# Kernel tuning notes

Measured on AMD Instinct MI355X. Metric: run time of the kernel, lower is better.

## Reference

```python
import jax, jax.numpy as jnp
import numpy as np

B, N, E = 2, 16000, 160000
NDIMS, NMEAS, NMODES = 2, 1, 128
IN_DIM, OUT_DIM, FC_DIM = 3, 1, 128
LAYERS = [64, 64, 64, 64]
INV_MIN, INV_MAX = 0.5, 2.0


def setup_inputs() -> dict:
    key = jax.random.key(0)
    ks = jax.random.split(key, 16)
    L = len(LAYERS) - 1
    C = LAYERS[0]
    scale = 1.0 / (C * C)
    u = lambda k, sh, s: jax.random.uniform(k, sh, jnp.float32, -s, s)
    inp = {}
    inp["x"] = jax.random.normal(ks[0], (B, N, IN_DIM), jnp.float32)
    inp["node_mask"] = jnp.ones((B, N, 1), jnp.int32)
    inp["nodes"] = jax.random.uniform(ks[1], (B, N, NDIMS), jnp.float32)
    inp["node_weights"] = jax.random.uniform(ks[2], (B, N, NMEAS), jnp.float32) / N
    inp["directed_edges"] = jax.random.randint(ks[3], (B, E, 2), 0, N, jnp.int32)
    inp["edge_gradient_weights"] = jax.random.normal(ks[4], (B, E, NDIMS), jnp.float32)
    inp["modes"] = jax.random.normal(ks[5], (NMODES, NDIMS, NMEAS), jnp.float32)
    # scaled_logit(1.0, 0.5, 2.0) = log(0.5/1.0)
    inp["inv_L_scale_latent"] = jnp.full((NDIMS, NMEAS), np.log((1.0 - INV_MIN) / (INV_MAX - 1.0)), jnp.float32)
    inp["fc0_W"] = u(ks[6], (C, IN_DIM), 1.0 / np.sqrt(IN_DIM))
    inp["fc0_b"] = jnp.zeros((C,), jnp.float32)
    inp["weights_c"] = u(ks[7], (L, C, C, NMODES, NMEAS), scale)
    inp["weights_s"] = u(ks[8], (L, C, C, NMODES, NMEAS), scale)
    inp["weights_0"] = u(ks[9], (L, C, C, 1, NMEAS), scale)
    inp["ws_W"] = u(ks[10], (L, C, C), 1.0 / np.sqrt(C))
    inp["ws_b"] = jnp.zeros((L, C), jnp.float32)
    inp["gws_W"] = u(ks[11], (L, C, C * NDIMS), 1.0 / np.sqrt(C * NDIMS))
    inp["gws_b"] = jnp.zeros((L, C), jnp.float32)
    inp["fc1_W"] = u(ks[12], (FC_DIM, C), 1.0 / np.sqrt(C))
    inp["fc1_b"] = jnp.zeros((FC_DIM,), jnp.float32)
    inp["fc2_W"] = u(ks[13], (OUT_DIM, FC_DIM), 1.0 / np.sqrt(FC_DIM))
    inp["fc2_b"] = jnp.zeros((OUT_DIM,), jnp.float32)
    return inp


def _forward(x, nodes, node_weights, edge_gradient_weights, modes, inv_L_scale_latent,
             fc0_W, fc0_b, weights_c, weights_s, weights_0, ws_W, ws_b, gws_W, gws_b,
             fc1_W, fc1_b, fc2_W, fc2_b, directed_edges):
    L = weights_c.shape[0]
    n = x.shape[1]
    # scaled sigmoid of latent inverse length scale
    inv_L = INV_MIN + (INV_MAX - INV_MIN) * jax.nn.sigmoid(inv_L_scale_latent)
    smodes = modes * inv_L  # [K, D, W]
    # Fourier bases over all nodes
    temp = jnp.einsum('bxd,kdw->bxkw', nodes, smodes)  # [B, N, K, W]
    bases_c, bases_s = jnp.cos(temp), jnp.sin(temp)
    bases_0 = jnp.ones(temp.shape[:2] + (1, temp.shape[-1]), temp.dtype)
    wnw = node_weights[:, :, None, :]  # [B, N, 1, W]
    wbases_c, wbases_s, wbases_0 = bases_c * wnw, bases_s * wnw, bases_0 * wnw

    tgt = directed_edges[..., 0]  # [B, E]
    src = directed_edges[..., 1]

    def grad_field(f):  # f: [B, C, N] -> [B, C*D, N]
        ft = jnp.transpose(f, (0, 2, 1))  # [B, N, C]
        f_src = jnp.take_along_axis(ft, src[..., None], axis=1)  # [B, E, C]
        f_tgt = jnp.take_along_axis(ft, tgt[..., None], axis=1)
        diff = f_src - f_tgt
        msg = jnp.einsum('bed,bec->becd', edge_gradient_weights, diff)  # [B, E, C, D]
        msg = msg.reshape(msg.shape[0], msg.shape[1], -1)  # [B, E, C*D]
        seg = jax.vmap(lambda m, t: jax.ops.segment_sum(m, t, num_segments=n))(msg, tgt)
        return jnp.transpose(seg, (0, 2, 1))  # [B, C*D, N]

    # lift: fc0 acts on channel dim
    h = jnp.einsum('oi,bni->bon', fc0_W, x) + fc0_b[None, :, None]  # [B, C, N]

    for i in range(L):
        # spectral conv with explicit bases
        x_c = jnp.einsum('bix,bxkw->bikw', h, wbases_c)
        x_s = -jnp.einsum('bix,bxkw->bikw', h, wbases_s)
        x_0 = jnp.einsum('bix,bxkw->bikw', h, wbases_0)
        f_c = jnp.einsum('bikw,iokw->bokw', x_c, weights_c[i]) - jnp.einsum('bikw,iokw->bokw', x_s, weights_s[i])
        f_s = jnp.einsum('bikw,iokw->bokw', x_s, weights_c[i]) + jnp.einsum('bikw,iokw->bokw', x_c, weights_s[i])
        f_0 = jnp.einsum('bikw,iokw->bokw', x_0, weights_0[i])
        x1 = (jnp.einsum('bokw,bxkw->box', f_0, bases_0)
              + 2 * jnp.einsum('bokw,bxkw->box', f_c, bases_c)
              - 2 * jnp.einsum('bokw,bxkw->box', f_s, bases_s))
        # pointwise linear W
        x2 = jnp.einsum('oi,bin->bon', ws_W[i], h) + ws_b[i][None, :, None]
        # differential operator D: gradient then linear
        x3 = jnp.einsum('oi,bin->bon', gws_W[i], grad_field(h)) + gws_b[i][None, :, None]
        h = x1 + x2 + x3
        if i < L - 1:
            h = jax.nn.gelu(h)

    out = jnp.transpose(h, (0, 2, 1))  # [B, N, C]
    out = jax.nn.gelu(jnp.einsum('oc,bnc->bno', fc1_W, out) + fc1_b)
    out = jnp.einsum('oc,bnc->bno', fc2_W, out) + fc2_b
    return out  # [B, N, out_dim]


def reference(x, node_mask, nodes, node_weights, directed_edges, edge_gradient_weights,
              modes, inv_L_scale_latent, fc0_W, fc0_b, weights_c, weights_s, weights_0,
              ws_W, ws_b, gws_W, gws_b, fc1_W, fc1_b, fc2_W, fc2_b):
    del node_mask  # padding mask; all-ones here, not used in the core math
    return _forward(x, nodes, node_weights, edge_gradient_weights, modes, inv_L_scale_latent,
                    fc0_W, fc0_b, weights_c, weights_s, weights_0, ws_W, ws_b, gws_W, gws_b,
                    fc1_W, fc1_b, fc2_W, fc2_b, directed_edges)
```

## Files before the change

### kernel.cpp

```cpp
#include <hip/hip_runtime.h>
#include <math.h>

#define BB 2
#define NN 16000
#define EE 160000
#define KK 128
#define CC 64
#define LL 3

typedef __attribute__((ext_vector_type(8))) short bf16x8;
typedef __attribute__((ext_vector_type(4))) float f32x4;

__device__ __forceinline__ float gelu_f(float x){
    float x3 = x * x * x;
    return 0.5f * x * (1.f + tanhf(0.7978845608028654f * (x + 0.044715f * x3)));
}
__device__ __forceinline__ ushort f2bf(float f){
    uint u = __float_as_uint(f);
    u += 0x7fff + ((u >> 16) & 1);
    return (ushort)(u >> 16);
}
__device__ __forceinline__ float bf2f(ushort h){ return __uint_as_float(((uint)h) << 16); }
__device__ __forceinline__ void fsplit(float v, ushort &hi, ushort &lo){
    hi = f2bf(v);
    lo = f2bf(v - bf2f(hi));
}
__device__ __forceinline__ uint pk2(ushort a, ushort b){ return (uint)a | ((uint)b << 16); }

__global__ __launch_bounds__(256) void k_bases(
    const float* __restrict__ nodes, const float* __restrict__ modes,
    const float* __restrict__ latent, const float* __restrict__ nw,
    ushort* __restrict__ cbh, ushort* __restrict__ cbl,
    ushort* __restrict__ sbh, ushort* __restrict__ sbl,
    ushort* __restrict__ wTh, ushort* __restrict__ wTl){
    int bid = blockIdx.x;
    int b = bid / 250, x0 = (bid % 250) * 64;
    int t = threadIdx.x;
    __shared__ float sm0[128], sm1[128], nwv[64];
    __shared__ uint tc[64][65], ts[64][65];
    if (t < 128){
        float i0 = 0.5f + 1.5f / (1.f + expf(-latent[0]));
        float i1 = 0.5f + 1.5f / (1.f + expf(-latent[1]));
        sm0[t] = modes[t*2+0] * i0;
        sm1[t] = modes[t*2+1] * i1;
    }
    if (t < 64) nwv[t] = nw[b*NN + x0 + t];
    __syncthreads();
    int xloc = t & 63;
    float n0 = nodes[((size_t)b*NN + x0 + xloc)*2 + 0];
    float n1 = nodes[((size_t)b*NN + x0 + xloc)*2 + 1];
    for (int kh = 0; kh < 2; kh++){
        int kq = t >> 6;
        #pragma unroll
        for (int j = 0; j < 16; j++){
            int kl = kq*16 + j;
            int k = kh*64 + kl;
            float tmp = n0*sm0[k] + n1*sm1[k];
            float sv, cv; sincosf(tmp, &sv, &cv);
            ushort h_, l_;
            fsplit(cv, h_, l_); tc[xloc][kl] = pk2(h_, l_);
            fsplit(sv, h_, l_); ts[xloc][kl] = pk2(h_, l_);
        }
        __syncthreads();
        {
            int q = t >> 6;
            size_t base = ((size_t)b*NN + x0 + xloc)*128 + kh*64 + q*16;
            #pragma unroll
            for (int g2 = 0; g2 < 2; g2++){
                uint u0 = tc[xloc][q*16 + g2*8 + 0], u1 = tc[xloc][q*16 + g2*8 + 1];
                uint u2 = tc[xloc][q*16 + g2*8 + 2], u3 = tc[xloc][q*16 + g2*8 + 3];
                uint u4 = tc[xloc][q*16 + g2*8 + 4], u5 = tc[xloc][q*16 + g2*8 + 5];
                uint u6 = tc[xloc][q*16 + g2*8 + 6], u7 = tc[xloc][q*16 + g2*8 + 7];
                uint4 vh, vl;
                vh.x = pk2((ushort)u0,(ushort)u1); vh.y = pk2((ushort)u2,(ushort)u3);
                vh.z = pk2((ushort)u4,(ushort)u5); vh.w = pk2((ushort)u6,(ushort)u7);
                vl.x = pk2((ushort)(u0>>16),(ushort)(u1>>16)); vl.y = pk2((ushort)(u2>>16),(ushort)(u3>>16));
                vl.z = pk2((ushort)(u4>>16),(ushort)(u5>>16)); vl.w = pk2((ushort)(u6>>16),(ushort)(u7>>16));
                *(uint4*)&cbh[base + g2*8] = vh;
                *(uint4*)&cbl[base + g2*8] = vl;
                u0 = ts[xloc][q*16 + g2*8 + 0]; u1 = ts[xloc][q*16 + g2*8 + 1];
                u2 = ts[xloc][q*16 + g2*8 + 2]; u3 = ts[xloc][q*16 + g2*8 + 3];
                u4 = ts[xloc][q*16 + g2*8 + 4]; u5 = ts[xloc][q*16 + g2*8 + 5];
                u6 = ts[xloc][q*16 + g2*8 + 6]; u7 = ts[xloc][q*16 + g2*8 + 7];
                vh.x = pk2((ushort)u0,(ushort)u1); vh.y = pk2((ushort)u2,(ushort)u3);
                vh.z = pk2((ushort)u4,(ushort)u5); vh.w = pk2((ushort)u6,(ushort)u7);
                vl.x = pk2((ushort)(u0>>16),(ushort)(u1>>16)); vl.y = pk2((ushort)(u2>>16),(ushort)(u3>>16));
                vl.z = pk2((ushort)(u4>>16),(ushort)(u5>>16)); vl.w = pk2((ushort)(u6>>16),(ushort)(u7>>16));
                *(uint4*)&sbh[base + g2*8] = vh;
                *(uint4*)&sbl[base + g2*8] = vl;
            }
        }
        {
            int k = t & 63, g = t >> 6;
            int kgc = kh*64 + k;
            int kgs = 128 + kh*64 + k;
            ushort hc[16], lc[16], hs[16], ls[16];
            #pragma unroll
            for (int j = 0; j < 16; j++){
                int xx = g*16 + j;
                float wgt = nwv[xx];
                uint uc = tc[xx][k], us = ts[xx][k];
                float vc = (bf2f((ushort)uc) + bf2f((ushort)(uc>>16))) * wgt;
                float vs = (bf2f((ushort)us) + bf2f((ushort)(us>>16))) * wgt;
                fsplit(vc, hc[j], lc[j]);
                fsplit(vs, hs[j], ls[j]);
            }
            size_t wbc = ((size_t)b*256 + kgc)*16000 + x0 + g*16;
            size_t wbs = ((size_t)b*256 + kgs)*16000 + x0 + g*16;
            uint4 v;
            v.x = pk2(hc[0],hc[1]); v.y = pk2(hc[2],hc[3]); v.z = pk2(hc[4],hc[5]); v.w = pk2(hc[6],hc[7]);
            *(uint4*)&wTh[wbc] = v;
            v.x = pk2(hc[8],hc[9]); v.y = pk2(hc[10],hc[11]); v.z = pk2(hc[12],hc[13]); v.w = pk2(hc[14],hc[15]);
            *(uint4*)&wTh[wbc + 8] = v;
            v.x = pk2(lc[0],lc[1]); v.y = pk2(lc[2],lc[3]); v.z = pk2(lc[4],lc[5]); v.w = pk2(lc[6],lc[7]);
            *(uint4*)&wTl[wbc] = v;
            v.x = pk2(lc[8],lc[9]); v.y = pk2(lc[10],lc[11]); v.z = pk2(lc[12],lc[13]); v.w = pk2(lc[14],lc[15]);
            *(uint4*)&wTl[wbc + 8] = v;
            v.x = pk2(hs[0],hs[1]); v.y = pk2(hs[2],hs[3]); v.z = pk2(hs[4],hs[5]); v.w = pk2(hs[6],hs[7]);
            *(uint4*)&wTh[wbs] = v;
            v.x = pk2(hs[8],hs[9]); v.y = pk2(hs[10],hs[11]); v.z = pk2(hs[12],hs[13]); v.w = pk2(hs[14],hs[15]);
            *(uint4*)&wTh[wbs + 8] = v;
            v.x = pk2(ls[0],ls[1]); v.y = pk2(ls[2],ls[3]); v.z = pk2(ls[4],ls[5]); v.w = pk2(ls[6],ls[7]);
            *(uint4*)&wTl[wbs] = v;
            v.x = pk2(ls[8],ls[9]); v.y = pk2(ls[10],ls[11]); v.z = pk2(ls[12],ls[13]); v.w = pk2(ls[14],ls[15]);
            *(uint4*)&wTl[wbs + 8] = v;
        }
        __syncthreads();
    }
}

__device__ __forceinline__ void write_h_outputs(
    const float* ot, const float* nws, int b, int s, int x0, int t, int doAux,
    float* __restrict__ hx, ushort* __restrict__ hxh, ushort* __restrict__ hxl,
    ushort* __restrict__ hwh, ushort* __restrict__ hwl, float* __restrict__ part0){
    {
        int xl = t >> 1, half = t & 1;
        size_t gb = ((size_t)b*NN + x0 + xl)*64 + half*32;
        const float* row = &ot[xl*68 + half*32];
        #pragma unroll
        for (int j = 0; j < 8; j++){
            float4 v; v.x = row[j*4]; v.y = row[j*4+1]; v.z = row[j*4+2]; v.w = row[j*4+3];
            *(float4*)&hx[gb + j*4] = v;
        }
        if (doAux){
            #pragma unroll
            for (int q = 0; q < 4; q++){
                ushort h_[8], l_[8];
                #pragma unroll
                for (int j = 0; j < 8; j++) fsplit(row[q*8 + j], h_[j], l_[j]);
                uint4 vh, vl;
                vh.x = pk2(h_[0],h_[1]); vh.y = pk2(h_[2],h_[3]); vh.z = pk2(h_[4],h_[5]); vh.w = pk2(h_[6],h_[7]);
                vl.x = pk2(l_[0],l_[1]); vl.y = pk2(l_[2],l_[3]); vl.z = pk2(l_[4],l_[5]); vl.w = pk2(l_[6],l_[7]);
                *(uint4*)&hxh[gb + q*8] = vh;
                *(uint4*)&hxl[gb + q*8] = vl;
            }
        }
    }
    if (doAux){
        int i = t & 63, g = t >> 6;
        float a = 0.f;
        #pragma unroll
        for (int rep = 0; rep < 4; rep++){
            int xs = g*32 + rep*8;
            ushort h_[8], l_[8];
            #pragma unroll
            for (int j = 0; j < 8; j++){
                float v = ot[(xs + j)*68 + i] * nws[xs + j];
                a += v;
                fsplit(v, h_[j], l_[j]);
            }
            uint4 vh, vl;
            vh.x = pk2(h_[0],h_[1]); vh.y = pk2(h_[2],h_[3]); vh.z = pk2(h_[4],h_[5]); vh.w = pk2(h_[6],h_[7]);
            vl.x = pk2(l_[0],l_[1]); vl.y = pk2(l_[2],l_[3]); vl.z = pk2(l_[4],l_[5]); vl.w = pk2(l_[6],l_[7]);
            size_t wb = (size_t)(b*64 + i)*16000 + x0 + xs;
            *(uint4*)&hwh[wb] = vh;
            *(uint4*)&hwl[wb] = vl;
        }
        part0[((size_t)(b*125 + s)*4 + g)*64 + i] = a;
    }
}

__global__ __launch_bounds__(256) void k_fc0(
    const float* __restrict__ x, const float* __restrict__ W,
    const float* __restrict__ bb, const float* __restrict__ nw,
    float* __restrict__ hx, ushort* __restrict__ hxh, ushort* __restrict__ hxl,
    ushort* __restrict__ hwh, ushort* __restrict__ hwl, float* __restrict__ part0){
    int bid = blockIdx.x;
    int b = bid / 125, s = bid % 125;
    int x0 = s * 128;
    int t = threadIdx.x;
    __shared__ float ot[128*68];
    __shared__ float nws[128];
    __shared__ float Wf[192], bf_[64];
    if (t < 192) Wf[t] = W[t];
    if (t < 64) bf_[t] = bb[t];
    if (t < 128) nws[t] = nw[b*NN + x0 + t];
    __syncthreads();
    {
        int xl = t >> 1, half = t & 1;
        float v0 = x[((size_t)b*NN + x0 + xl)*3 + 0];
        float v1 = x[((size_t)b*NN + x0 + xl)*3 + 1];
        float v2 = x[((size_t)b*NN + x0 + xl)*3 + 2];
        #pragma unroll
        for (int j = 0; j < 32; j++){
            int o = half*32 + j;
            ot[xl*68 + o] = Wf[o*3]*v0 + Wf[o*3+1]*v1 + Wf[o*3+2]*v2 + bf_[o];
        }
    }
    __syncthreads();
    write_h_outputs(ot, nws, b, s, x0, t, 1, hx, hxh, hxl, hwh, hwl, part0);
}

__global__ __launch_bounds__(256) void csr_hist(
    const int* __restrict__ edges, int* __restrict__ cnt){
    int idx = blockIdx.x * 256 + threadIdx.x;
    if (idx >= BB*EE) return;
    int b = idx / EE;
    int tgt = edges[(size_t)idx*2];
    atomicAdd(&cnt[b*NN + tgt], 1);
}

__global__ __launch_bounds__(1024) void csr_scan(
    const int* __restrict__ cnt, int* __restrict__ rowptr, int* __restrict__ cursor){
    int b = blockIdx.x;
    int t = threadIdx.x;
    __shared__ int lds[1024];
    int base = t * 16;
    int v[16];
    int run = 0;
    #pragma unroll
    for (int j = 0; j < 16; j++){
        int n = base + j;
        int c = (n < NN) ? cnt[b*NN + n] : 0;
        v[j] = run;
        run += c;
    }
    lds[t] = run;
    __syncthreads();
    for (int off = 1; off < 1024; off <<= 1){
        int xv = (t >= off) ? lds[t-off] : 0;
        __syncthreads();
        lds[t] += xv;
        __syncthreads();
    }
    int toff = lds[t] - run;
    #pragma unroll
    for (int j = 0; j < 16; j++){
        int n = base + j;
        if (n < NN){
            int p = toff + v[j];
            rowptr[b*(NN+1) + n] = p;
            cursor[b*NN + n] = p;
        }
    }
    if (t == 1023) rowptr[b*(NN+1) + NN] = lds[1023];
}

__global__ __launch_bounds__(256) void csr_fill(
    const int* __restrict__ edges, const float* __restrict__ egw,
    int* __restrict__ cursor, int* __restrict__ insrc, float2* __restrict__ inw){
    int idx = blockIdx.x * 256 + threadIdx.x;
    if (idx >= BB*EE) return;
    int b = idx / EE;
    int tgt = edges[(size_t)idx*2];
    int src = edges[(size_t)idx*2 + 1];
    int pos = atomicAdd(&cursor[b*NN + tgt], 1);
    insrc[(size_t)b*EE + pos] = src;
    const float2 wv = *(const float2*)&egw[(size_t)idx*2];
    inw[(size_t)b*EE + pos] = wv;
}

__global__ __launch_bounds__(256) void k1_fwd(
    const ushort* __restrict__ hwH, const ushort* __restrict__ hwL,
    const ushort* __restrict__ wTH, const ushort* __restrict__ wTL,
    float* __restrict__ part){
    int bid = blockIdx.x;
    int b = bid / 250, s = bid % 250;
    int x0 = s * 64;
    int t = threadIdx.x, l = t & 63, w = t >> 6;
    __shared__ __align__(16) ushort Bh[128*64], Bl[128*64];
    f32x4 acc[16] = {};
    bf16x8 Ah[2], Al[2];
    int i = w*16 + (l & 15);
    #pragma unroll
    for (int ks = 0; ks < 2; ks++){
        size_t ab = (size_t)(b*64 + i)*16000 + x0 + ks*32 + ((l >> 4) * 8);
        Ah[ks] = *reinterpret_cast<const bf16x8*>(&hwH[ab]);
        Al[ks] = *reinterpret_cast<const bf16x8*>(&hwL[ab]);
    }
    for (int p = 0; p < 2; p++){
        #pragma unroll
        for (int it = 0; it < 4; it++){
            int u = it*256 + t;
            int kloc = u >> 3, q = u & 7;
            size_t g = ((size_t)(b*256 + p*128 + kloc))*16000 + x0 + q*8;
            uint4 vh = *(const uint4*)&wTH[g];
            uint4 vl = *(const uint4*)&wTL[g];
            int ldsb = kloc*128 + ((q*16) ^ ((kloc & 7) << 4));
            *(uint4*)&Bh[ldsb >> 1] = vh;
            *(uint4*)&Bl[ldsb >> 1] = vl;
        }
        __syncthreads();
        #pragma unroll
        for (int kt = 0; kt < 8; kt++){
            int kcol = kt*16 + (l & 15);
            int ai = p*8 + kt;
            #pragma unroll
            for (int ks = 0; ks < 2; ks++){
                int boff = kcol*128 + (((ks*64) + ((l >> 4) * 16)) ^ ((kcol & 7) << 4));
                bf16x8 bh = *reinterpret_cast<const bf16x8*>(&Bh[boff >> 1]);
                bf16x8 bl = *reinterpret_cast<const bf16x8*>(&Bl[boff >> 1]);
                acc[ai] = __builtin_amdgcn_mfma_f32_16x16x32_bf16(Ah[ks], bh, acc[ai], 0, 0, 0);
                acc[ai] = __builtin_amdgcn_mfma_f32_16x16x32_bf16(Ah[ks], bl, acc[ai], 0, 0, 0);
                acc[ai] = __builtin_amdgcn_mfma_f32_16x16x32_bf16(Al[ks], bh, acc[ai], 0, 0, 0);
            }
        }
        __syncthreads();
    }
    size_t pb = (size_t)(b*250 + s) * 64 * 256;
    #pragma unroll
    for (int nt = 0; nt < 16; nt++){
        #pragma unroll
        for (int r = 0; r < 4; r++){
            int irow = w*16 + (l >> 4)*4 + r;
            part[pb + (size_t)irow*256 + nt*16 + (l & 15)] = acc[nt][r];
        }
    }
}

__global__ __launch_bounds__(512) void k1_reduce(
    const float* __restrict__ part, float* __restrict__ Sc, float* __restrict__ Ss){
    int b = blockIdx.x >> 6, i = blockIdx.x & 63;
    int t = threadIdx.x;
    int c = t & 255, sh = t >> 8;
    float a0=0,a1=0,a2=0,a3=0;
    int j = sh;
    for (; j + 6 < 250; j += 8){
        a0 += part[((size_t)(b*250 + j    )*64 + i)*256 + c];
        a1 += part[((size_t)(b*250 + j + 2)*64 + i)*256 + c];
        a2 += part[((size_t)(b*250 + j + 4)*64 + i)*256 + c];
        a3 += part[((size_t)(b*250 + j + 6)*64 + i)*256 + c];
    }
    for (; j < 250; j += 2)
        a0 += part[((size_t)(b*250 + j)*64 + i)*256 + c];
    float sum = (a0+a1)+(a2+a3);
    __shared__ float r2[256];
    if (sh) r2[c] = sum;
    __syncthreads();
    if (!sh){
        sum += r2[c];
        if (c < 128) Sc[(size_t)(b*64 + i)*128 + c] = sum;
        else         Ss[(size_t)(b*64 + i)*128 + (c - 128)] = sum;
    }
}

__global__ __launch_bounds__(256) void k2_mix(
    const float* __restrict__ Sc, const float* __restrict__ Ss,
    const float* __restrict__ part0,
    const float* __restrict__ wc, const float* __restrict__ wsp,
    const float* __restrict__ w0,
    const float* __restrict__ wsb, const float* __restrict__ gwsb,
    const float* __restrict__ wsW, const float* __restrict__ gwsW,
    ushort* __restrict__ WbH, ushort* __restrict__ WbL,
    float* __restrict__ bias, int l){
    int b = blockIdx.x >> 6, o = blockIdx.x & 63;
    int t = threadIdx.x;
    __shared__ float fc2s[2][128], fs2s[2][128];
    __shared__ float red[64];
    if (t < 64){
        float x0 = 0.f;
        for (int s2 = 0; s2 < 500; s2++) x0 += part0[(size_t)(b*500 + s2)*64 + t];
        red[t] = x0 * w0[((size_t)l*CC + t)*CC + o];
    }
    int k = t & 127, hf = t >> 7;
    float fc = 0.f, fs = 0.f;
    for (int i = hf*32; i < hf*32 + 32; i++){
        float sc = Sc[(size_t)(b*CC + i)*KK + k];
        float ss = Ss[(size_t)(b*CC + i)*KK + k];
        size_t wi = (((size_t)l*CC + i)*CC + o)*KK + k;
        float a = wc[wi], bb2 = wsp[wi];
        fc += sc*a + ss*bb2;
        fs += sc*bb2 - ss*a;
    }
    fc2s[hf][k] = fc; fs2s[hf][k] = fs;
    __syncthreads();
    size_t wb = (size_t)(b*CC + o) * 448;
    if (t < 128){
        float FC = fc2s[0][t] + fc2s[1][t];
        float FS = fs2s[0][t] + fs2s[1][t];
        ushort h_, l_;
        fsplit(2.f*FC, h_, l_);
        WbH[wb + t] = h_; WbL[wb + t] = l_;
        fsplit(-2.f*FS, h_, l_);
        WbH[wb + 128 + t] = h_; WbL[wb + 128 + t] = l_;
    }
    if (t < 192){
        float v = (t < 64) ? wsW[((size_t)l*CC + o)*CC + t]
                           : gwsW[((size_t)l*CC + o)*128 + (t - 64)];
        ushort h_, l_; fsplit(v, h_, l_);
        WbH[wb + 256 + t] = h_; WbL[wb + 256 + t] = l_;
    }
    if (t == 0){
        float f0 = 0.f;
        for (int i = 0; i < 64; i++) f0 += red[i];
        bias[b*CC + o] = f0 + wsb[l*CC + o] + gwsb[l*CC + o];
    }
}

__global__ __launch_bounds__(256) void k_grad(
    const float* __restrict__ h, const int* __restrict__ rowptr,
    const int* __restrict__ insrc, const float2* __restrict__ inw,
    ushort* __restrict__ segh, ushort* __restrict__ segl){
    int bid = blockIdx.x;
    int b = bid / 2000, n0 = (bid % 2000) * 8;
    int w = threadIdx.x >> 6, c = threadIdx.x & 63;
    const float*  hb  = h + (size_t)b*NN*CC;
    const int*    isb = insrc + (size_t)b*EE;
    const float2* iwb = inw + (size_t)b*EE;
    #pragma unroll
    for (int g = 0; g < 2; g++){
        int n = n0 + w*2 + g;
        float hn = hb[(size_t)n*CC + c];
        int p0 = rowptr[b*(NN+1) + n];
        int p1 = rowptr[b*(NN+1) + n + 1];
        float a0 = 0.f, a1 = 0.f;
        int p = p0;
        for (; p + 4 <= p1; p += 4){
            int s0 = isb[p], s1 = isb[p+1], s2 = isb[p+2], s3 = isb[p+3];
            float2 w0 = iwb[p], w1 = iwb[p+1], w2 = iwb[p+2], w3 = iwb[p+3];
            float d0 = hb[(size_t)s0*CC + c] - hn;
            float d1 = hb[(size_t)s1*CC + c] - hn;
            float d2 = hb[(size_t)s2*CC + c] - hn;
            float d3 = hb[(size_t)s3*CC + c] - hn;
            a0 += w0.x*d0 + w1.x*d1 + w2.x*d2 + w3.x*d3;
            a1 += w0.y*d0 + w1.y*d1 + w2.y*d2 + w3.y*d3;
        }
        for (; p < p1; p++){
            int sx = isb[p]; float2 ww = iwb[p];
            float d = hb[(size_t)sx*CC + c] - hn;
            a0 += ww.x*d; a1 += ww.y*d;
        }
        ushort h0_, l0_, h1_, l1_;
        fsplit(a0, h0_, l0_);
        fsplit(a1, h1_, l1_);
        size_t sb2 = ((size_t)b*NN + n)*128 + 2*c;
        *(uint*)&segh[sb2] = pk2(h0_, h1_);
        *(uint*)&segl[sb2] = pk2(l0_, l1_);
    }
}

__global__ __launch_bounds__(256) void k3_gemm(
    const ushort* __restrict__ WbH, const ushort* __restrict__ WbL,
    const float* __restrict__ bias,
    const ushort* __restrict__ cbh, const ushort* __restrict__ cbl,
    const ushort* __restrict__ sbh, const ushort* __restrict__ sbl,
    const ushort* __restrict__ hxh, const ushort* __restrict__ hxl,
    const ushort* __restrict__ sgh, const ushort* __restrict__ sgl,
    const float* __restrict__ nw,
    float* __restrict__ hxO, ushort* __restrict__ hxhO, ushort* __restrict__ hxlO,
    ushort* __restrict__ hwhO, ushort* __restrict__ hwlO, float* __restrict__ part0,
    int doAux){
    int bid = blockIdx.x;
    int b = bid / 125, s = bid % 125, x0 = s * 128;
    int t = threadIdx.x, l = t & 63, w = t >> 6;
    __shared__ __align__(16) char smem[34816];
    ushort* Vh = (ushort*)smem;
    ushort* Vl = Vh + 8192;
    __shared__ float nws[128];
    if (t < 128) nws[t] = nw[b*NN + x0 + t];
    f32x4 acc[8] = {};
    int o = w*16 + (l & 15);
    for (int cc = 0; cc < 7; cc++){
        const ushort *srcH, *srcL; int rl, co;
        switch (cc){
            case 0:  srcH = cbh; srcL = cbl; rl = 128; co = 0;  break;
            case 1:  srcH = cbh; srcL = cbl; rl = 128; co = 64; break;
            case 2:  srcH = sbh; srcL = sbl; rl = 128; co = 0;  break;
            case 3:  srcH = sbh; srcL = sbl; rl = 128; co = 64; break;
            case 4:  srcH = hxh; srcL = hxl; rl = 64;  co = 0;  break;
            case 5:  srcH = sgh; srcL = sgl; rl = 128; co = 0;  break;
            default: srcH = sgh; srcL = sgl; rl = 128; co = 64; break;
        }
        __syncthreads();
        #pragma unroll
        for (int it = 0; it < 4; it++){
            int u = it*256 + t;
            int xl2 = u >> 3, q = u & 7;
            size_t g = (size_t)(b*NN + x0 + xl2)*rl + co + q*8;
            uint4 vh = *(const uint4*)&srcH[g];
            uint4 vl2 = *(const uint4*)&srcL[g];
            int ldsb = xl2*128 + ((q*16) ^ ((xl2 & 7) << 4));
            *(uint4*)&Vh[ldsb >> 1] = vh;
            *(uint4*)&Vl[ldsb >> 1] = vl2;
        }
        __syncthreads();
        bf16x8 Ah[2], Al[2];
        #pragma unroll
        for (int ks = 0; ks < 2; ks++){
            size_t ab = (size_t)(b*64 + o)*448 + cc*64 + ks*32 + ((l >> 4) * 8);
            Ah[ks] = *reinterpret_cast<const bf16x8*>(&WbH[ab]);
            Al[ks] = *reinterpret_cast<const bf16x8*>(&WbL[ab]);
        }
        #pragma unroll
        for (int nt = 0; nt < 8; nt++){
            int xc = nt*16 + (l & 15);
            #pragma unroll
            for (int ks = 0; ks < 2; ks++){
                int boff = xc*128 + (((ks*64) + ((l >> 4) * 16)) ^ ((xc & 7) << 4));
                bf16x8 bh = *reinterpret_cast<const bf16x8*>(&Vh[boff >> 1]);
                bf16x8 bl = *reinterpret_cast<const bf16x8*>(&Vl[boff >> 1]);
                acc[nt] = __builtin_amdgcn_mfma_f32_16x16x32_bf16(Ah[ks], bh, acc[nt], 0, 0, 0);
                acc[nt] = __builtin_amdgcn_mfma_f32_16x16x32_bf16(Ah[ks], bl, acc[nt], 0, 0, 0);
                acc[nt] = __builtin_amdgcn_mfma_f32_16x16x32_bf16(Al[ks], bh, acc[nt], 0, 0, 0);
            }
        }
    }
    __syncthreads();
    float* ot = (float*)smem;
    float bv[4];
    #pragma unroll
    for (int r = 0; r < 4; r++) bv[r] = bias[b*64 + w*16 + (l >> 4)*4 + r];
    #pragma unroll
    for (int nt = 0; nt < 8; nt++){
        int xc = nt*16 + (l & 15);
        #pragma unroll
        for (int r = 0; r < 4; r++){
            float v = acc[nt][r] + bv[r];
            if (doAux) v = gelu_f(v);
            ot[xc*68 + (w*16 + (l >> 4)*4 + r)] = v;
        }
    }
    __syncthreads();
    write_h_outputs(ot, nws, b, s, x0, t, doAux, hxO, hxhO, hxlO, hwhO, hwlO, part0);
}

__global__ __launch_bounds__(256) void k_head(
    const float* __restrict__ h, const float* __restrict__ W1,
    const float* __restrict__ b1, const float* __restrict__ W2,
    const float* __restrict__ b2, float* __restrict__ out){
    int bid = blockIdx.x;
    int b = bid / 250, n0 = (bid % 250) * 64;
    int t = threadIdx.x, w = t >> 6, f = t & 63;
    __shared__ float Wl[128][65];
    #pragma unroll
    for (int r = 0; r < 8; r++){
        int u = r*256 + t;
        int ff = u >> 4, cq = u & 15;
        float4 v = *(const float4*)&W1[ff*64 + cq*4];
        Wl[ff][cq*4+0] = v.x; Wl[ff][cq*4+1] = v.y;
        Wl[ff][cq*4+2] = v.z; Wl[ff][cq*4+3] = v.w;
    }
    __syncthreads();
    float w2a = W2[f], w2b = W2[64+f];
    float b1a = b1[f], b1b = b1[64+f];
    float b2v = b2[0];
    for (int g = 0; g < 16; g++){
        int n = n0 + w*16 + g;
        float hv = h[((size_t)b*NN + n)*CC + f];
        float a1 = b1a, a2 = b1b;
        #pragma unroll
        for (int c2 = 0; c2 < 64; c2++){
            float xv = __shfl(hv, c2, 64);
            a1 += Wl[f][c2] * xv;
            a2 += Wl[64+f][c2] * xv;
        }
        float p = gelu_f(a1)*w2a + gelu_f(a2)*w2b;
        for (int off = 32; off; off >>= 1) p += __shfl_down(p, off, 64);
        if (f == 0) out[(size_t)b*NN + n] = p + b2v;
    }
}

extern "C" void kernel_launch(void* const* d_in, const int* in_sizes, int n_in,
                              void* d_out, int out_size, void* d_ws, size_t ws_size,
                              hipStream_t stream){
    const float* x_in  = (const float*)d_in[0];
    const float* nodes = (const float*)d_in[2];
    const float* nw    = (const float*)d_in[3];
    const int*   edges = (const int*)d_in[4];
    const float* egw   = (const float*)d_in[5];
    const float* modes = (const float*)d_in[6];
    const float* latent= (const float*)d_in[7];
    const float* fc0W  = (const float*)d_in[8];
    const float* fc0b  = (const float*)d_in[9];
    const float* wc    = (const float*)d_in[10];
    const float* wsp   = (const float*)d_in[11];
    const float* w0    = (const float*)d_in[12];
    const float* wsW   = (const float*)d_in[13];
    const float* wsb   = (const float*)d_in[14];
    const float* gwsW  = (const float*)d_in[15];
    const float* gwsb  = (const float*)d_in[16];
    const float* fc1W  = (const float*)d_in[17];
    const float* fc1b  = (const float*)d_in[18];
    const float* fc2W  = (const float*)d_in[19];
    const float* fc2b  = (const float*)d_in[20];
    float* out = (float*)d_out;

    char* wsbase = (char*)d_ws;
    size_t off = 0;
    auto alloc = [&](size_t bytes) -> void* {
        void* p = wsbase + off;
        off += (bytes + 255) & ~(size_t)255;
        return p;
    };
    ushort* cbh = (ushort*)alloc((size_t)BB*NN*128*2);
    ushort* cbl = (ushort*)alloc((size_t)BB*NN*128*2);
    ushort* sbh = (ushort*)alloc((size_t)BB*NN*128*2);
    ushort* sbl = (ushort*)alloc((size_t)BB*NN*128*2);
    ushort* wTh = (ushort*)alloc((size_t)BB*256*NN*2);
    ushort* wTl = (ushort*)alloc((size_t)BB*256*NN*2);
    float*  hx[2];  ushort* hxh[2]; ushort* hxl[2]; ushort* hwh[2]; ushort* hwl[2];
    for (int i = 0; i < 2; i++){
        hx[i]  = (float*) alloc((size_t)BB*NN*64*4);
        hxh[i] = (ushort*)alloc((size_t)BB*NN*64*2);
        hxl[i] = (ushort*)alloc((size_t)BB*NN*64*2);
        hwh[i] = (ushort*)alloc((size_t)BB*64*NN*2);
        hwl[i] = (ushort*)alloc((size_t)BB*64*NN*2);
    }
    ushort* segh = (ushort*)alloc((size_t)BB*NN*128*2);
    ushort* segl = (ushort*)alloc((size_t)BB*NN*128*2);
    float*  part = (float*) alloc((size_t)BB*250*64*256*4);
    float*  part0= (float*) alloc((size_t)BB*125*4*64*4);
    float*  Sc   = (float*) alloc((size_t)BB*64*128*4);
    float*  Ss   = (float*) alloc((size_t)BB*64*128*4);
    ushort* WbH  = (ushort*)alloc((size_t)BB*64*448*2);
    ushort* WbL  = (ushort*)alloc((size_t)BB*64*448*2);
    float*  bias = (float*) alloc((size_t)BB*64*4);
    int*   cnt   = (int*)   alloc((size_t)BB*NN*4);
    int*   rowptr= (int*)   alloc((size_t)BB*(NN+4)*4);
    int*   cursor= (int*)   alloc((size_t)BB*NN*4);
    int*   insrc = (int*)   alloc((size_t)BB*EE*4);
    float2* inw  = (float2*)alloc((size_t)BB*EE*8);

    k_bases<<<BB*250, 256, 0, stream>>>(nodes, modes, latent, nw,
                                        cbh, cbl, sbh, sbl, wTh, wTl);
    k_fc0<<<BB*125, 256, 0, stream>>>(x_in, fc0W, fc0b, nw,
                                      hx[0], hxh[0], hxl[0], hwh[0], hwl[0], part0);

    hipMemsetAsync(cnt, 0, (size_t)BB*NN*4, stream);
    csr_hist<<<(BB*EE+255)/256, 256, 0, stream>>>(edges, cnt);
    csr_scan<<<BB, 1024, 0, stream>>>(cnt, rowptr, cursor);
    csr_fill<<<(BB*EE+255)/256, 256, 0, stream>>>(edges, egw, cursor, insrc, inw);

    int cur = 0;
    for (int l = 0; l < LL; l++){
        int nxt = cur ^ 1;
        int doAux = (l < LL-1) ? 1 : 0;
        k1_fwd<<<BB*250, 256, 0, stream>>>(hwh[cur], hwl[cur], wTh, wTl, part);
        k1_reduce<<<BB*64, 512, 0, stream>>>(part, Sc, Ss);
        k2_mix<<<BB*64, 256, 0, stream>>>(Sc, Ss, part0, wc, wsp, w0, wsb, gwsb,
                                          wsW, gwsW, WbH, WbL, bias, l);
        k_grad<<<BB*2000, 256, 0, stream>>>(hx[cur], rowptr, insrc, inw, segh, segl);
        k3_gemm<<<BB*125, 256, 0, stream>>>(WbH, WbL, bias,
                                            cbh, cbl, sbh, sbl,
                                            hxh[cur], hxl[cur], segh, segl, nw,
                                            hx[nxt], hxh[nxt], hxl[nxt],
                                            hwh[nxt], hwl[nxt], part0, doAux);
        cur = nxt;
    }
    k_head<<<BB*250, 256, 0, stream>>>(hx[cur], fc1W, fc1b, fc2W, fc2b, out);
    (void)in_sizes; (void)n_in; (void)out_size; (void)ws_size; (void)segh; (void)segl;
}
```

Baseline: 509.2 us.

## Drop low-order bf16 split for Fourier bases and spectral forward GEMM

Stores the sin/cos bases and the weighted transposed bases as single bf16 values instead of hi/lo pairs. The spectral forward GEMM then runs one MFMA per step instead of three, and the bases part of the output GEMM skips the low-order loads and products. The aim is to cut memory traffic and MFMA work in the per-layer k1_fwd and k3_gemm kernels, at the cost of reduced accuracy in the spectral transforms. Node weights are no longer folded into wT, and the k1_reduce and k2_mix parallelism is also reworked.

```diff
diff --git a/kernel.cpp b/kernel.cpp
--- a/kernel.cpp
+++ b/kernel.cpp
@@ -29,14 +29,13 @@
 
 __global__ __launch_bounds__(256) void k_bases(
     const float* __restrict__ nodes, const float* __restrict__ modes,
-    const float* __restrict__ latent, const float* __restrict__ nw,
-    ushort* __restrict__ cbh, ushort* __restrict__ cbl,
-    ushort* __restrict__ sbh, ushort* __restrict__ sbl,
-    ushort* __restrict__ wTh, ushort* __restrict__ wTl){
+    const float* __restrict__ latent,
+    ushort* __restrict__ cbh, ushort* __restrict__ sbh,
+    ushort* __restrict__ wTh){
     int bid = blockIdx.x;
     int b = bid / 250, x0 = (bid % 250) * 64;
     int t = threadIdx.x;
-    __shared__ float sm0[128], sm1[128], nwv[64];
+    __shared__ float sm0[128], sm1[128];
     __shared__ uint tc[64][65], ts[64][65];
     if (t < 128){
         float i0 = 0.5f + 1.5f / (1.f + expf(-latent[0]));
@@ -44,7 +43,6 @@
         sm0[t] = modes[t*2+0] * i0;
         sm1[t] = modes[t*2+1] * i1;
     }
-    if (t < 64) nwv[t] = nw[b*NN + x0 + t];
     __syncthreads();
     int xloc = t & 63;
     float n0 = nodes[((size_t)b*NN + x0 + xloc)*2 + 0];
@@ -57,9 +55,8 @@
             int k = kh*64 + kl;
             float tmp = n0*sm0[k] + n1*sm1[k];
             float sv, cv; sincosf(tmp, &sv, &cv);
-            ushort h_, l_;
-            fsplit(cv, h_, l_); tc[xloc][kl] = pk2(h_, l_);
-            fsplit(sv, h_, l_); ts[xloc][kl] = pk2(h_, l_);
+            tc[xloc][kl] = (uint)f2bf(cv);
+            ts[xloc][kl] = (uint)f2bf(sv);
         }
         __syncthreads();
         {
@@ -71,39 +68,29 @@
                 uint u2 = tc[xloc][q*16 + g2*8 + 2], u3 = tc[xloc][q*16 + g2*8 + 3];
                 uint u4 = tc[xloc][q*16 + g2*8 + 4], u5 = tc[xloc][q*16 + g2*8 + 5];
                 uint u6 = tc[xloc][q*16 + g2*8 + 6], u7 = tc[xloc][q*16 + g2*8 + 7];
-                uint4 vh, vl;
+                uint4 vh;
                 vh.x = pk2((ushort)u0,(ushort)u1); vh.y = pk2((ushort)u2,(ushort)u3);
                 vh.z = pk2((ushort)u4,(ushort)u5); vh.w = pk2((ushort)u6,(ushort)u7);
-                vl.x = pk2((ushort)(u0>>16),(ushort)(u1>>16)); vl.y = pk2((ushort)(u2>>16),(ushort)(u3>>16));
-                vl.z = pk2((ushort)(u4>>16),(ushort)(u5>>16)); vl.w = pk2((ushort)(u6>>16),(ushort)(u7>>16));
                 *(uint4*)&cbh[base + g2*8] = vh;
-                *(uint4*)&cbl[base + g2*8] = vl;
                 u0 = ts[xloc][q*16 + g2*8 + 0]; u1 = ts[xloc][q*16 + g2*8 + 1];
                 u2 = ts[xloc][q*16 + g2*8 + 2]; u3 = ts[xloc][q*16 + g2*8 + 3];
                 u4 = ts[xloc][q*16 + g2*8 + 4]; u5 = ts[xloc][q*16 + g2*8 + 5];
                 u6 = ts[xloc][q*16 + g2*8 + 6]; u7 = ts[xloc][q*16 + g2*8 + 7];
                 vh.x = pk2((ushort)u0,(ushort)u1); vh.y = pk2((ushort)u2,(ushort)u3);
                 vh.z = pk2((ushort)u4,(ushort)u5); vh.w = pk2((ushort)u6,(ushort)u7);
-                vl.x = pk2((ushort)(u0>>16),(ushort)(u1>>16)); vl.y = pk2((ushort)(u2>>16),(ushort)(u3>>16));
-                vl.z = pk2((ushort)(u4>>16),(ushort)(u5>>16)); vl.w = pk2((ushort)(u6>>16),(ushort)(u7>>16));
                 *(uint4*)&sbh[base + g2*8] = vh;
-                *(uint4*)&sbl[base + g2*8] = vl;
             }
         }
         {
             int k = t & 63, g = t >> 6;
             int kgc = kh*64 + k;
             int kgs = 128 + kh*64 + k;
-            ushort hc[16], lc[16], hs[16], ls[16];
+            ushort hc[16], hs[16];
             #pragma unroll
             for (int j = 0; j < 16; j++){
                 int xx = g*16 + j;
-                float wgt = nwv[xx];
-                uint uc = tc[xx][k], us = ts[xx][k];
-                float vc = (bf2f((ushort)uc) + bf2f((ushort)(uc>>16))) * wgt;
-                float vs = (bf2f((ushort)us) + bf2f((ushort)(us>>16))) * wgt;
-                fsplit(vc, hc[j], lc[j]);
-                fsplit(vs, hs[j], ls[j]);
+                hc[j] = (ushort)tc[xx][k];
+                hs[j] = (ushort)ts[xx][k];
             }
             size_t wbc = ((size_t)b*256 + kgc)*16000 + x0 + g*16;
             size_t wbs = ((size_t)b*256 + kgs)*16000 + x0 + g*16;
@@ -112,18 +99,10 @@
             *(uint4*)&wTh[wbc] = v;
             v.x = pk2(hc[8],hc[9]); v.y = pk2(hc[10],hc[11]); v.z = pk2(hc[12],hc[13]); v.w = pk2(hc[14],hc[15]);
             *(uint4*)&wTh[wbc + 8] = v;
-            v.x = pk2(lc[0],lc[1]); v.y = pk2(lc[2],lc[3]); v.z = pk2(lc[4],lc[5]); v.w = pk2(lc[6],lc[7]);
-            *(uint4*)&wTl[wbc] = v;
-            v.x = pk2(lc[8],lc[9]); v.y = pk2(lc[10],lc[11]); v.z = pk2(lc[12],lc[13]); v.w = pk2(lc[14],lc[15]);
-            *(uint4*)&wTl[wbc + 8] = v;
             v.x = pk2(hs[0],hs[1]); v.y = pk2(hs[2],hs[3]); v.z = pk2(hs[4],hs[5]); v.w = pk2(hs[6],hs[7]);
             *(uint4*)&wTh[wbs] = v;
             v.x = pk2(hs[8],hs[9]); v.y = pk2(hs[10],hs[11]); v.z = pk2(hs[12],hs[13]); v.w = pk2(hs[14],hs[15]);
             *(uint4*)&wTh[wbs + 8] = v;
-            v.x = pk2(ls[0],ls[1]); v.y = pk2(ls[2],ls[3]); v.z = pk2(ls[4],ls[5]); v.w = pk2(ls[6],ls[7]);
-            *(uint4*)&wTl[wbs] = v;
-            v.x = pk2(ls[8],ls[9]); v.y = pk2(ls[10],ls[11]); v.z = pk2(ls[12],ls[13]); v.w = pk2(ls[14],ls[15]);
-            *(uint4*)&wTl[wbs + 8] = v;
         }
         __syncthreads();
     }
@@ -132,7 +111,7 @@
 __device__ __forceinline__ void write_h_outputs(
     const float* ot, const float* nws, int b, int s, int x0, int t, int doAux,
     float* __restrict__ hx, ushort* __restrict__ hxh, ushort* __restrict__ hxl,
-    ushort* __restrict__ hwh, ushort* __restrict__ hwl, float* __restrict__ part0){
+    ushort* __restrict__ hwh, float* __restrict__ part0){
     {
         int xl = t >> 1, half = t & 1;
         size_t gb = ((size_t)b*NN + x0 + xl)*64 + half*32;
@@ -162,19 +141,17 @@
         #pragma unroll
         for (int rep = 0; rep < 4; rep++){
             int xs = g*32 + rep*8;
-            ushort h_[8], l_[8];
+            ushort h_[8];
             #pragma unroll
             for (int j = 0; j < 8; j++){
                 float v = ot[(xs + j)*68 + i] * nws[xs + j];
                 a += v;
-                fsplit(v, h_[j], l_[j]);
+                h_[j] = f2bf(v);
             }
-            uint4 vh, vl;
+            uint4 vh;
             vh.x = pk2(h_[0],h_[1]); vh.y = pk2(h_[2],h_[3]); vh.z = pk2(h_[4],h_[5]); vh.w = pk2(h_[6],h_[7]);
-            vl.x = pk2(l_[0],l_[1]); vl.y = pk2(l_[2],l_[3]); vl.z = pk2(l_[4],l_[5]); vl.w = pk2(l_[6],l_[7]);
             size_t wb = (size_t)(b*64 + i)*16000 + x0 + xs;
             *(uint4*)&hwh[wb] = vh;
-            *(uint4*)&hwl[wb] = vl;
         }
         part0[((size_t)(b*125 + s)*4 + g)*64 + i] = a;
     }
@@ -184,7 +161,7 @@
     const float* __restrict__ x, const float* __restrict__ W,
     const float* __restrict__ bb, const float* __restrict__ nw,
     float* __restrict__ hx, ushort* __restrict__ hxh, ushort* __restrict__ hxl,
-    ushort* __restrict__ hwh, ushort* __restrict__ hwl, float* __restrict__ part0){
+    ushort* __restrict__ hwh, float* __restrict__ part0){
     int bid = blockIdx.x;
     int b = bid / 125, s = bid % 125;
     int x0 = s * 128;
@@ -208,7 +185,7 @@
         }
     }
     __syncthreads();
-    write_h_outputs(ot, nws, b, s, x0, t, 1, hx, hxh, hxl, hwh, hwl, part0);
+    write_h_outputs(ot, nws, b, s, x0, t, 1, hx, hxh, hxl, hwh, part0);
 }
 
 __global__ __launch_bounds__(256) void csr_hist(
@@ -271,34 +248,32 @@
 }
 
 __global__ __launch_bounds__(256) void k1_fwd(
-    const ushort* __restrict__ hwH, const ushort* __restrict__ hwL,
-    const ushort* __restrict__ wTH, const ushort* __restrict__ wTL,
+    const ushort* __restrict__ hwH,
+    const ushort* __restrict__ wTH,
     float* __restrict__ part){
     int bid = blockIdx.x;
     int b = bid / 250, s = bid % 250;
     int x0 = s * 64;
     int t = threadIdx.x, l = t & 63, w = t >> 6;
-    __shared__ __align__(16) ushort Bh[128*64], Bl[128*64];
+    __shared__ __align__(16) ushort Bh[128*64];
     f32x4 acc[16] = {};
-    bf16x8 Ah[2], Al[2];
+    bf16x8 Ah[2];
     int i = w*16 + (l & 15);
     #pragma unroll
     for (int ks = 0; ks < 2; ks++){
         size_t ab = (size_t)(b*64 + i)*16000 + x0 + ks*32 + ((l >> 4) * 8);
         Ah[ks] = *reinterpret_cast<const bf16x8*>(&hwH[ab]);
-        Al[ks] = *reinterpret_cast<const bf16x8*>(&hwL[ab]);
     }
     for (int p = 0; p < 2; p++){
+        if (p) __syncthreads();
         #pragma unroll
         for (int it = 0; it < 4; it++){
             int u = it*256 + t;
             int kloc = u >> 3, q = u & 7;
             size_t g = ((size_t)(b*256 + p*128 + kloc))*16000 + x0 + q*8;
             uint4 vh = *(const uint4*)&wTH[g];
-            uint4 vl = *(const uint4*)&wTL[g];
             int ldsb = kloc*128 + ((q*16) ^ ((kloc & 7) << 4));
             *(uint4*)&Bh[ldsb >> 1] = vh;
-            *(uint4*)&Bl[ldsb >> 1] = vl;
         }
         __syncthreads();
         #pragma unroll
@@ -309,13 +284,9 @@
             for (int ks = 0; ks < 2; ks++){
                 int boff = kcol*128 + (((ks*64) + ((l >> 4) * 16)) ^ ((kcol & 7) << 4));
                 bf16x8 bh = *reinterpret_cast<const bf16x8*>(&Bh[boff >> 1]);
-                bf16x8 bl = *reinterpret_cast<const bf16x8*>(&Bl[boff >> 1]);
                 acc[ai] = __builtin_amdgcn_mfma_f32_16x16x32_bf16(Ah[ks], bh, acc[ai], 0, 0, 0);
-                acc[ai] = __builtin_amdgcn_mfma_f32_16x16x32_bf16(Ah[ks], bl, acc[ai], 0, 0, 0);
-                acc[ai] = __builtin_amdgcn_mfma_f32_16x16x32_bf16(Al[ks], bh, acc[ai], 0, 0, 0);
             }
         }
-        __syncthreads();
     }
     size_t pb = (size_t)(b*250 + s) * 64 * 256;
     #pragma unroll
@@ -328,27 +299,29 @@
     }
 }
 
-__global__ __launch_bounds__(512) void k1_reduce(
+__global__ __launch_bounds__(256) void k1_reduce(
     const float* __restrict__ part, float* __restrict__ Sc, float* __restrict__ Ss){
-    int b = blockIdx.x >> 6, i = blockIdx.x & 63;
+    int bid = blockIdx.x;
+    int b = bid >> 7, rr = bid & 127;
+    int i = rr >> 1, half = rr & 1;
     int t = threadIdx.x;
-    int c = t & 255, sh = t >> 8;
+    int c = half*128 + (t & 127), sh = t >> 7;
+    const float* pb = part + ((size_t)b*16000 + i)*256 + c;
     float a0=0,a1=0,a2=0,a3=0;
     int j = sh;
     for (; j + 6 < 250; j += 8){
-        a0 += part[((size_t)(b*250 + j    )*64 + i)*256 + c];
-        a1 += part[((size_t)(b*250 + j + 2)*64 + i)*256 + c];
-        a2 += part[((size_t)(b*250 + j + 4)*64 + i)*256 + c];
-        a3 += part[((size_t)(b*250 + j + 6)*64 + i)*256 + c];
-    }
-    for (; j < 250; j += 2)
-        a0 += part[((size_t)(b*250 + j)*64 + i)*256 + c];
+        a0 += pb[(size_t)(j    )*16384];
+        a1 += pb[(size_t)(j + 2)*16384];
+        a2 += pb[(size_t)(j + 4)*16384];
+        a3 += pb[(size_t)(j + 6)*16384];
+    }
+    for (; j < 250; j += 2) a0 += pb[(size_t)j*16384];
     float sum = (a0+a1)+(a2+a3);
-    __shared__ float r2[256];
-    if (sh) r2[c] = sum;
+    __shared__ float r2[128];
+    if (sh) r2[t & 127] = sum;
     __syncthreads();
     if (!sh){
-        sum += r2[c];
+        sum += r2[t & 127];
         if (c < 128) Sc[(size_t)(b*64 + i)*128 + c] = sum;
         else         Ss[(size_t)(b*64 + i)*128 + (c - 128)] = sum;
     }
@@ -366,11 +339,14 @@
     int b = blockIdx.x >> 6, o = blockIdx.x & 63;
     int t = threadIdx.x;
     __shared__ float fc2s[2][128], fs2s[2][128];
+    __shared__ float redp[4][64];
     __shared__ float red[64];
-    if (t < 64){
-        float x0 = 0.f;
-        for (int s2 = 0; s2 < 500; s2++) x0 += part0[(size_t)(b*500 + s2)*64 + t];
-        red[t] = x0 * w0[((size_t)l*CC + t)*CC + o];
+    {
+        int i = t & 63, grp = t >> 6;
+        float a = 0.f;
+        for (int s2 = grp; s2 < 500; s2 += 4)
+            a += part0[(size_t)(b*500 + s2)*64 + i];
+        redp[grp][i] = a;
     }
     int k = t & 127, hf = t >> 7;
     float fc = 0.f, fs = 0.f;
@@ -384,6 +360,8 @@
     }
     fc2s[hf][k] = fc; fs2s[hf][k] = fs;
     __syncthreads();
+    if (t < 64)
+        red[t] = (redp[0][t]+redp[1][t]+redp[2][t]+redp[3][t]) * w0[((size_t)l*CC + t)*CC + o];
     size_t wb = (size_t)(b*CC + o) * 448;
     if (t < 128){
         float FC = fc2s[0][t] + fc2s[1][t];
@@ -394,12 +372,19 @@
         fsplit(-2.f*FS, h_, l_);
         WbH[wb + 128 + t] = h_; WbL[wb + 128 + t] = l_;
     }
-    if (t < 192){
-        float v = (t < 64) ? wsW[((size_t)l*CC + o)*CC + t]
-                           : gwsW[((size_t)l*CC + o)*128 + (t - 64)];
+    if (t >= 128 && t < 192){
+        int q = t - 128;
+        float v = wsW[((size_t)l*CC + o)*CC + q];
         ushort h_, l_; fsplit(v, h_, l_);
-        WbH[wb + 256 + t] = h_; WbL[wb + 256 + t] = l_;
-    }
+        WbH[wb + 256 + q] = h_; WbL[wb + 256 + q] = l_;
+    }
+    if (t >= 128){
+        int q = t - 128;
+        float v = gwsW[((size_t)l*CC + o)*128 + q];
+        ushort h_, l_; fsplit(v, h_, l_);
+        WbH[wb + 320 + q] = h_; WbL[wb + 320 + q] = l_;
+    }
+    __syncthreads();
     if (t == 0){
         float f0 = 0.f;
         for (int i = 0; i < 64; i++) f0 += red[i];
@@ -452,13 +437,12 @@
 __global__ __launch_bounds__(256) void k3_gemm(
     const ushort* __restrict__ WbH, const ushort* __restrict__ WbL,
     const float* __restrict__ bias,
-    const ushort* __restrict__ cbh, const ushort* __restrict__ cbl,
-    const ushort* __restrict__ sbh, const ushort* __restrict__ sbl,
+    const ushort* __restrict__ cbh, const ushort* __restrict__ sbh,
     const ushort* __restrict__ hxh, const ushort* __restrict__ hxl,
     const ushort* __restrict__ sgh, const ushort* __restrict__ sgl,
     const float* __restrict__ nw,
     float* __restrict__ hxO, ushort* __restrict__ hxhO, ushort* __restrict__ hxlO,
-    ushort* __restrict__ hwhO, ushort* __restrict__ hwlO, float* __restrict__ part0,
+    ushort* __restrict__ hwhO, float* __restrict__ part0,
     int doAux){
     int bid = blockIdx.x;
     int b = bid / 125, s = bid % 125, x0 = s * 128;
@@ -471,15 +455,15 @@
     f32x4 acc[8] = {};
     int o = w*16 + (l & 15);
     for (int cc = 0; cc < 7; cc++){
-        const ushort *srcH, *srcL; int rl, co;
+        const ushort *srcH, *srcL; int rl, co, lo;
         switch (cc){
-            case 0:  srcH = cbh; srcL = cbl; rl = 128; co = 0;  break;
-            case 1:  srcH = cbh; srcL = cbl; rl = 128; co = 64; break;
-            case 2:  srcH = sbh; srcL = sbl; rl = 128; co = 0;  break;
-            case 3:  srcH = sbh; srcL = sbl; rl = 128; co = 64; break;
-            case 4:  srcH = hxh; srcL = hxl; rl = 64;  co = 0;  break;
-            case 5:  srcH = sgh; srcL = sgl; rl = 128; co = 0;  break;
-            default: srcH = sgh; srcL = sgl; rl = 128; co = 64; break;
+            case 0:  srcH = cbh; srcL = cbh; rl = 128; co = 0;  lo = 0; break;
+            case 1:  srcH = cbh; srcL = cbh; rl = 128; co = 64; lo = 0; break;
+            case 2:  srcH = sbh; srcL = sbh; rl = 128; co = 0;  lo = 0; break;
+            case 3:  srcH = sbh; srcL = sbh; rl = 128; co = 64; lo = 0; break;
+            case 4:  srcH = hxh; srcL = hxl; rl = 64;  co = 0;  lo = 1; break;
+            case 5:  srcH = sgh; srcL = sgl; rl = 128; co = 0;  lo = 1; break;
+            default: srcH = sgh; srcL = sgl; rl = 128; co = 64; lo = 1; break;
         }
         __syncthreads();
         #pragma unroll
@@ -488,10 +472,12 @@
             int xl2 = u >> 3, q = u & 7;
             size_t g = (size_t)(b*NN + x0 + xl2)*rl + co + q*8;
             uint4 vh = *(const uint4*)&srcH[g];
-            uint4 vl2 = *(const uint4*)&srcL[g];
             int ldsb = xl2*128 + ((q*16) ^ ((xl2 & 7) << 4));
             *(uint4*)&Vh[ldsb >> 1] = vh;
-            *(uint4*)&Vl[ldsb >> 1] = vl2;
+            if (lo){
+                uint4 vl2 = *(const uint4*)&srcL[g];
+                *(uint4*)&Vl[ldsb >> 1] = vl2;
+            }
         }
         __syncthreads();
         bf16x8 Ah[2], Al[2];
@@ -508,10 +494,12 @@
             for (int ks = 0; ks < 2; ks++){
                 int boff = xc*128 + (((ks*64) + ((l >> 4) * 16)) ^ ((xc & 7) << 4));
                 bf16x8 bh = *reinterpret_cast<const bf16x8*>(&Vh[boff >> 1]);
-                bf16x8 bl = *reinterpret_cast<const bf16x8*>(&Vl[boff >> 1]);
                 acc[nt] = __builtin_amdgcn_mfma_f32_16x16x32_bf16(Ah[ks], bh, acc[nt], 0, 0, 0);
-                acc[nt] = __builtin_amdgcn_mfma_f32_16x16x32_bf16(Ah[ks], bl, acc[nt], 0, 0, 0);
-                acc[nt] = __builtin_amdgcn_mfma_f32_16x16x32_bf16(Al[ks], bh, acc[nt], 0, 0, 0);
+                if (lo){
+                    bf16x8 bl = *reinterpret_cast<const bf16x8*>(&Vl[boff >> 1]);
+                    acc[nt] = __builtin_amdgcn_mfma_f32_16x16x32_bf16(Ah[ks], bl, acc[nt], 0, 0, 0);
+                    acc[nt] = __builtin_amdgcn_mfma_f32_16x16x32_bf16(Al[ks], bh, acc[nt], 0, 0, 0);
+                }
             }
         }
     }
@@ -531,7 +519,7 @@
         }
     }
     __syncthreads();
-    write_h_outputs(ot, nws, b, s, x0, t, doAux, hxO, hxhO, hxlO, hwhO, hwlO, part0);
+    write_h_outputs(ot, nws, b, s, x0, t, doAux, hxO, hxhO, hxlO, hwhO, part0);
 }
 
 __global__ __launch_bounds__(256) void k_head(
@@ -603,18 +591,14 @@
         return p;
     };
     ushort* cbh = (ushort*)alloc((size_t)BB*NN*128*2);
-    ushort* cbl = (ushort*)alloc((size_t)BB*NN*128*2);
     ushort* sbh = (ushort*)alloc((size_t)BB*NN*128*2);
-    ushort* sbl = (ushort*)alloc((size_t)BB*NN*128*2);
     ushort* wTh = (ushort*)alloc((size_t)BB*256*NN*2);
-    ushort* wTl = (ushort*)alloc((size_t)BB*256*NN*2);
-    float*  hx[2];  ushort* hxh[2]; ushort* hxl[2]; ushort* hwh[2]; ushort* hwl[2];
+    float*  hx[2];  ushort* hxh[2]; ushort* hxl[2]; ushort* hwh[2];
     for (int i = 0; i < 2; i++){
         hx[i]  = (float*) alloc((size_t)BB*NN*64*4);
         hxh[i] = (ushort*)alloc((size_t)BB*NN*64*2);
         hxl[i] = (ushort*)alloc((size_t)BB*NN*64*2);
         hwh[i] = (ushort*)alloc((size_t)BB*64*NN*2);
-        hwl[i] = (ushort*)alloc((size_t)BB*64*NN*2);
     }
     ushort* segh = (ushort*)alloc((size_t)BB*NN*128*2);
     ushort* segl = (ushort*)alloc((size_t)BB*NN*128*2);
@@ -631,10 +615,9 @@
     int*   insrc = (int*)   alloc((size_t)BB*EE*4);
     float2* inw  = (float2*)alloc((size_t)BB*EE*8);
 
-    k_bases<<<BB*250, 256, 0, stream>>>(nodes, modes, latent, nw,
-                                        cbh, cbl, sbh, sbl, wTh, wTl);
+    k_bases<<<BB*250, 256, 0, stream>>>(nodes, modes, latent, cbh, sbh, wTh);
     k_fc0<<<BB*125, 256, 0, stream>>>(x_in, fc0W, fc0b, nw,
-                                      hx[0], hxh[0], hxl[0], hwh[0], hwl[0], part0);
+                                      hx[0], hxh[0], hxl[0], hwh[0], part0);
 
     hipMemsetAsync(cnt, 0, (size_t)BB*NN*4, stream);
     csr_hist<<<(BB*EE+255)/256, 256, 0, stream>>>(edges, cnt);
@@ -645,18 +628,18 @@
     for (int l = 0; l < LL; l++){
         int nxt = cur ^ 1;
         int doAux = (l < LL-1) ? 1 : 0;
-        k1_fwd<<<BB*250, 256, 0, stream>>>(hwh[cur], hwl[cur], wTh, wTl, part);
-        k1_reduce<<<BB*64, 512, 0, stream>>>(part, Sc, Ss);
+        k1_fwd<<<BB*250, 256, 0, stream>>>(hwh[cur], wTh, part);
+        k1_reduce<<<BB*128, 256, 0, stream>>>(part, Sc, Ss);
         k2_mix<<<BB*64, 256, 0, stream>>>(Sc, Ss, part0, wc, wsp, w0, wsb, gwsb,
                                           wsW, gwsW, WbH, WbL, bias, l);
         k_grad<<<BB*2000, 256, 0, stream>>>(hx[cur], rowptr, insrc, inw, segh, segl);
         k3_gemm<<<BB*125, 256, 0, stream>>>(WbH, WbL, bias,
-                                            cbh, cbl, sbh, sbl,
+                                            cbh, sbh,
                                             hxh[cur], hxl[cur], segh, segl, nw,
                                             hx[nxt], hxh[nxt], hxl[nxt],
-                                            hwh[nxt], hwl[nxt], part0, doAux);
+                                            hwh[nxt], part0, doAux);
         cur = nxt;
     }
     k_head<<<BB*250, 256, 0, stream>>>(hx[cur], fc1W, fc1b, fc2W, fc2b, out);
-    (void)in_sizes; (void)n_in; (void)out_size; (void)ws_size; (void)segh; (void)segl;
-}
+    (void)in_sizes; (void)n_in; (void)out_size; (void)ws_size;
+}
```

Measured after the change: 552.9 us. 8.6% more time.
